# Performance work log

Hardware: AMD Instinct MI355X
Metric: run time of the kernel (lower is better)

Reference implementation:

```python
import jax, jax.numpy as jnp
import numpy as np

B, S, H = 32, 2048, 1024

def setup_inputs() -> dict:
    key = jax.random.key(0)
    k1, k2, k3, k4 = jax.random.split(key, 4)
    scale_w = 1.0 / np.sqrt(3 * H)
    scale_v = 1.0 / np.sqrt(H)
    return {
        "enc_output": jax.random.normal(k1, (B, S, 2 * H), dtype=jnp.float32),
        "enc_mask": jnp.ones((B, S, 1), dtype=jnp.float32),
        "dec_hidden": jax.random.normal(k2, (1, B, H), dtype=jnp.float32),
        "W_w": jax.random.normal(k3, (H, 3 * H), dtype=jnp.float32) * scale_w,
        "W_b": jnp.zeros((H,), dtype=jnp.float32),
        "V_w": jax.random.normal(k4, (1, H), dtype=jnp.float32) * scale_v,
        "V_b": jnp.zeros((1,), dtype=jnp.float32),
    }


def reference(enc_output, enc_mask, dec_hidden, W_w, W_b, V_w, V_b):
    # enc_output: (B, S, 2H); enc_mask: (B, S, 1); dec_hidden: (1, B, H)
    b, s, _ = enc_output.shape
    h = dec_hidden.shape[-1]
    dec = jnp.broadcast_to(jnp.transpose(dec_hidden, (1, 0, 2)), (b, s, h))  # (B,S,H)
    x = jnp.concatenate([enc_output, dec], axis=-1)                          # (B,S,3H)
    energy = jnp.tanh(jnp.einsum('bsk,hk->bsh', x, W_w) + W_b)               # (B,S,H)
    scores = jnp.einsum('bsh,oh->bso', energy, V_w)[..., 0] + V_b[0]         # (B,S)
    keep = enc_mask[..., 0] > 0  # original masks where (1 - mask) is True
    scores = jnp.where(keep, scores, -jnp.inf)
    attn = jax.nn.softmax(scores, axis=-1)                                   # (B,S)
    context = jnp.einsum('bs,bsd->bd', attn, enc_output)                     # (B,2H)
    return context
```

## Files before the change

### kernel.cpp

```cpp
#include <hip/hip_runtime.h>
#include <hip/hip_bf16.h>
#include <math.h>

#define B_   32
#define S_   2048
#define H_   1024
#define K2H  2048
#define M_TOT (B_*S_)

typedef __attribute__((ext_vector_type(8))) short bf16x8;
typedef __attribute__((ext_vector_type(4))) float f32x4;

__device__ __forceinline__ short f2bf(float f) {
    union { float f; unsigned u; } c; c.f = f;
    unsigned u = c.u;
    unsigned r = u + 0x7FFFu + ((u >> 16) & 1u);
    return (short)(r >> 16);
}

__device__ __forceinline__ void bar() {
    asm volatile("" ::: "memory");
    __builtin_amdgcn_s_barrier();
    asm volatile("" ::: "memory");
}

__device__ __forceinline__ void gload16(const short* g, short* l) {
    __builtin_amdgcn_global_load_lds(
        (const __attribute__((address_space(1))) void*)g,
        (__attribute__((address_space(3))) void*)l,
        16, 0, 0);
}

__global__ void prep_kernel(const float* __restrict__ enc, short* __restrict__ encb,
                            const float* __restrict__ Ww, short* __restrict__ w1,
                            const float* __restrict__ dec, const float* __restrict__ Wb,
                            float* __restrict__ dproj) {
    int bid = blockIdx.x;
    int t = threadIdx.x;
    if (bid < 65536) {
        size_t e = ((size_t)bid * 256 + t) * 8;
        float4 v0 = *reinterpret_cast<const float4*>(enc + e);
        float4 v1 = *reinterpret_cast<const float4*>(enc + e + 4);
        short s[8];
        s[0]=f2bf(v0.x); s[1]=f2bf(v0.y); s[2]=f2bf(v0.z); s[3]=f2bf(v0.w);
        s[4]=f2bf(v1.x); s[5]=f2bf(v1.y); s[6]=f2bf(v1.z); s[7]=f2bf(v1.w);
        *reinterpret_cast<int4*>(encb + e) = *reinterpret_cast<const int4*>(s);
    } else if (bid < 65536 + 2048) {
        int idx = (bid - 65536) * 256 + t;
        int e = idx * 4;
        int h = e >> 11;
        int k = e & 2047;
        float4 v = *reinterpret_cast<const float4*>(Ww + (size_t)h * 3072 + k);
        short4 o;
        o.x = f2bf(v.x); o.y = f2bf(v.y); o.z = f2bf(v.z); o.w = f2bf(v.w);
        *reinterpret_cast<short4*>(w1 + (size_t)h * 2048 + k) = o;
    } else {
        __shared__ float dl[1024];
        int db = bid - 65536 - 2048;
        int b = db >> 4;
        int hc = db & 15;
        for (int i = t; i < 1024; i += 256) dl[i] = dec[b * 1024 + i];
        __syncthreads();
        int wv = t >> 6, lane = t & 63;
        for (int it = 0; it < 16; ++it) {
            int h = hc * 64 + wv * 16 + it;
            const float* wrow = Ww + (size_t)h * 3072 + 2048;
            float acc = 0.f;
            for (int j = lane; j < 1024; j += 64) acc += dl[j] * wrow[j];
            for (int m = 32; m >= 1; m >>= 1) acc += __shfl_xor(acc, m);
            if (lane == 0) dproj[b * 1024 + h] = acc + Wb[h];
        }
    }
}

#define NT_ 64

#define STAGE(dst, src, T) do { \
    _Pragma("unroll") \
    for (int u = 0; u < 2; ++u) { \
        int lr = u * 128 + sr; \
        int cs = (sc ^ ((lr >> 1) & 3)) * 8; \
        gload16((src) + (size_t)lr * K2H + (T) * 32 + cs, (dst) + lr * 32 + sc * 8); \
    } } while (0)

#define RDA(dstf, AS, roff) do { \
    _Pragma("unroll") \
    for (int ii = 0; ii < 4; ++ii) { \
        int R = wm * 128 + (roff) + ii * 16 + (lane & 15); \
        dstf[ii] = *reinterpret_cast<const bf16x8*>(&(AS)[R * 32 + (((lane >> 4) ^ ((R >> 1) & 3)) * 8)]); \
    } } while (0)

#define RDB(dstf, BS) do { \
    _Pragma("unroll") \
    for (int jj = 0; jj < 4; ++jj) { \
        int R = wn * 64 + jj * 16 + (lane & 15); \
        dstf[jj] = *reinterpret_cast<const bf16x8*>(&(BS)[R * 32 + (((lane >> 4) ^ ((R >> 1) & 3)) * 8)]); \
    } } while (0)

#define TILE(T, AS, BS, APF, BPF) do { \
    RDA(aF, AS, 0); \
    RDB(bF, BS); \
    RDA(aG, AS, 64); \
    if ((T) + 3 < NT_) { STAGE(APF, abase, (T) + 3); STAGE(BPF, bbase, (T) + 3); } \
    if ((T) <= NT_ - 4)      { asm volatile("s_waitcnt vmcnt(8)" ::: "memory"); } \
    else if ((T) == NT_ - 3) { asm volatile("s_waitcnt vmcnt(4)" ::: "memory"); } \
    else if ((T) == NT_ - 2) { asm volatile("s_waitcnt vmcnt(0)" ::: "memory"); } \
    bar(); \
    __builtin_amdgcn_s_setprio(1); \
    _Pragma("unroll") for (int ii = 0; ii < 4; ++ii) \
      _Pragma("unroll") for (int jj = 0; jj < 4; ++jj) \
        acc[ii][jj] = __builtin_amdgcn_mfma_f32_16x16x32_bf16(aF[ii], bF[jj], acc[ii][jj], 0, 0, 0); \
    _Pragma("unroll") for (int ii = 0; ii < 4; ++ii) \
      _Pragma("unroll") for (int jj = 0; jj < 4; ++jj) \
        acc[4+ii][jj] = __builtin_amdgcn_mfma_f32_16x16x32_bf16(aG[ii], bF[jj], acc[4+ii][jj], 0, 0, 0); \
    __builtin_amdgcn_s_setprio(0); \
    bar(); \
} while (0)

__launch_bounds__(512, 1)
__global__ void fused_gemm8(const short* __restrict__ encb, const short* __restrict__ w1,
                            const float* __restrict__ dproj, const float* __restrict__ Vw,
                            float* __restrict__ scores_p) {
    __shared__ short A0[8192], A1[8192], A2[8192], A3[8192];
    __shared__ short B0[8192], B1[8192], B2[8192], B3[8192];
    int bid = blockIdx.x;
    int x = bid & 7, r = bid >> 3;
    int nt = r & 3;
    int mt = ((r >> 2) << 3) | x;
    int m0 = mt * 256, n0 = nt * 256;
    int t5 = threadIdx.x, lane = t5 & 63, wv = t5 >> 6;
    int wm = wv >> 2, wn = wv & 3;

    int sr = t5 >> 2;
    int sc = t5 & 3;
    const short* abase = encb + (size_t)m0 * K2H;
    const short* bbase = w1 + (size_t)n0 * K2H;

    f32x4 acc[8][4] = {};
    bf16x8 aF[4], aG[4], bF[4];

    STAGE(A0, abase, 0); STAGE(B0, bbase, 0);
    STAGE(A1, abase, 1); STAGE(B1, bbase, 1);
    STAGE(A2, abase, 2); STAGE(B2, bbase, 2);
    asm volatile("s_waitcnt vmcnt(8)" ::: "memory");
    bar();

    for (int to = 0; to < NT_ / 4; ++to) {
        int T = to * 4;
        TILE(T,     A0, B0, A3, B3);
        TILE(T + 1, A1, B1, A0, B0);
        TILE(T + 2, A2, B2, A1, B1);
        TILE(T + 3, A3, B3, A2, B2);
    }

    int b = m0 >> 11;
    float dp[4], vvv[4];
#pragma unroll
    for (int j = 0; j < 4; ++j) {
        int hg = n0 + wn * 64 + j * 16 + (lane & 15);
        dp[j] = dproj[b * 1024 + hg];
        vvv[j] = Vw[hg];
    }
    float* sp = scores_p + (size_t)(nt * 4 + wn) * M_TOT;
#pragma unroll
    for (int i = 0; i < 8; ++i) {
#pragma unroll
        for (int q = 0; q < 4; ++q) {
            float part = 0.f;
#pragma unroll
            for (int j = 0; j < 4; ++j)
                part += vvv[j] * tanhf(acc[i][j][q] + dp[j]);
            part += __shfl_xor(part, 1);
            part += __shfl_xor(part, 2);
            part += __shfl_xor(part, 4);
            part += __shfl_xor(part, 8);
            if ((lane & 15) == 0) {
                int mg = m0 + wm * 128 + i * 16 + ((lane >> 4) << 2) + q;
                sp[mg] = part;
            }
        }
    }
}

__global__ void softmax_kernel(const float* __restrict__ scores_p, const float* __restrict__ mask,
                               float* __restrict__ attn) {
    int b = blockIdx.x;
    int t = threadIdx.x;
    __shared__ float red[8];
    __shared__ float red2[8];
    float v[8];
    float mx = -INFINITY;
#pragma unroll
    for (int k = 0; k < 8; ++k) {
        int s = t + k * 256;
        float xv = 0.f;
#pragma unroll
        for (int p = 0; p < 16; ++p) xv += scores_p[(size_t)p * M_TOT + b * 2048 + s];
        float mk = mask[b * 2048 + s];
        xv = (mk > 0.f) ? xv : -INFINITY;
        v[k] = xv;
        mx = fmaxf(mx, xv);
    }
    int lane = t & 63, wv = t >> 6;
    for (int m = 32; m >= 1; m >>= 1) mx = fmaxf(mx, __shfl_xor(mx, m));
    if (lane == 0) red[wv] = mx;
    __syncthreads();
    mx = fmaxf(fmaxf(red[0], red[1]), fmaxf(red[2], red[3]));
    float sum = 0.f;
#pragma unroll
    for (int k = 0; k < 8; ++k) { v[k] = __expf(v[k] - mx); sum += v[k]; }
    for (int m = 32; m >= 1; m >>= 1) sum += __shfl_xor(sum, m);
    if (lane == 0) red2[wv] = sum;
    __syncthreads();
    sum = red2[0] + red2[1] + red2[2] + red2[3];
    float inv = 1.f / sum;
#pragma unroll
    for (int k = 0; k < 8; ++k) attn[b * 2048 + t + k * 256] = v[k] * inv;
}

#define SCH 64
__global__ void context_kernel(const short* __restrict__ encb, const float* __restrict__ attn,
                               float* __restrict__ out) {
    int bid = blockIdx.x;
    int b = bid >> 5;
    int schunk = bid & 31;
    int t = threadIdx.x;
    __shared__ float aw[SCH];
    if (t < SCH) aw[t] = attn[b * 2048 + schunk * SCH + t];
    __syncthreads();
    int c = t * 8;
    const short* base = encb + (size_t)b * S_ * K2H + (size_t)(schunk * SCH) * K2H + c;
    float acc[8] = {};
    for (int s = 0; s < SCH; ++s) {
        float w = aw[s];
        bf16x8 v = *reinterpret_cast<const bf16x8*>(base + (size_t)s * K2H);
#pragma unroll
        for (int j = 0; j < 8; ++j) {
            union { unsigned u; float f; } cv;
            cv.u = ((unsigned)(unsigned short)v[j]) << 16;
            acc[j] += w * cv.f;
        }
    }
    float* o = out + b * 2048 + c;
#pragma unroll
    for (int j = 0; j < 8; ++j) atomicAdd(o + j, acc[j]);
}

extern "C" void kernel_launch(void* const* d_in, const int* in_sizes, int n_in,
                              void* d_out, int out_size, void* d_ws, size_t ws_size,
                              hipStream_t stream) {
    const float* enc  = (const float*)d_in[0];
    const float* mask = (const float*)d_in[1];
    const float* dec  = (const float*)d_in[2];
    const float* Ww   = (const float*)d_in[3];
    const float* Wb   = (const float*)d_in[4];
    const float* Vw   = (const float*)d_in[5];
    float* out = (float*)d_out;

    char* ws = (char*)d_ws;
    const size_t ENC_B = (size_t)M_TOT * K2H * 2;
    short* encb     = (short*)ws;
    short* w1       = (short*)(ws + ENC_B);
    float* scores_p = (float*)(ws + ENC_B + (4u << 20));
    float* dproj    = (float*)(ws + ENC_B + (8u << 20));
    float* attn     = (float*)(ws + ENC_B + (8u << 20) + (128u << 10));

    hipMemsetAsync(out, 0, (size_t)out_size * sizeof(float), stream);

    prep_kernel<<<68096, 256, 0, stream>>>(enc, encb, Ww, w1, dec, Wb, dproj);
    fused_gemm8<<<1024, 512, 0, stream>>>(encb, w1, dproj, Vw, scores_p);
    softmax_kernel<<<32, 256, 0, stream>>>(scores_p, mask, attn);
    context_kernel<<<1024, 256, 0, stream>>>(encb, attn, out);
}
```

Before: 648.8 us.

## Interleave GEMM main loop into four MFMA phases with triple-buffered LDS

Restructures the bf16 GEMM main loop so each K-tile is split into four MFMA quadrants, with LDS fragment reads and global-to-LDS stage loads interleaved between barriers. The prefetch depth drops from three tiles ahead with four LDS buffers to two tiles ahead with three buffers, which cuts LDS usage. The aim is finer-grained overlap of memory traffic with MFMA work. The cost is more barriers per tile and less latency hiding from the shallower prefetch.

Result: slower. 679.6 us (+4.7%).

```diff
diff --git a/kernel.cpp b/kernel.cpp
--- a/kernel.cpp
+++ b/kernel.cpp
@@ -75,13 +75,11 @@
 
 #define NT_ 64
 
-#define STAGE(dst, src, T) do { \
-    _Pragma("unroll") \
-    for (int u = 0; u < 2; ++u) { \
-        int lr = u * 128 + sr; \
-        int cs = (sc ^ ((lr >> 1) & 3)) * 8; \
-        gload16((src) + (size_t)lr * K2H + (T) * 32 + cs, (dst) + lr * 32 + sc * 8); \
-    } } while (0)
+#define STAGE1(dst, src, T, RB) do { \
+    int gr_ = (RB) + sr; \
+    gload16((src) + (size_t)gr_ * K2H + (T) * 32 + ((sc ^ ((gr_ >> 1) & 3)) * 8), \
+            (dst) + gr_ * 32 + sc * 8); \
+  } while (0)
 
 #define RDA(dstf, AS, roff) do { \
     _Pragma("unroll") \
@@ -90,39 +88,48 @@
         dstf[ii] = *reinterpret_cast<const bf16x8*>(&(AS)[R * 32 + (((lane >> 4) ^ ((R >> 1) & 3)) * 8)]); \
     } } while (0)
 
-#define RDB(dstf, BS) do { \
+#define RDB2(dstf, BS, coff) do { \
     _Pragma("unroll") \
-    for (int jj = 0; jj < 4; ++jj) { \
-        int R = wn * 64 + jj * 16 + (lane & 15); \
+    for (int jj = 0; jj < 2; ++jj) { \
+        int R = wn * 64 + (coff) + jj * 16 + (lane & 15); \
         dstf[jj] = *reinterpret_cast<const bf16x8*>(&(BS)[R * 32 + (((lane >> 4) ^ ((R >> 1) & 3)) * 8)]); \
     } } while (0)
 
-#define TILE(T, AS, BS, APF, BPF) do { \
-    RDA(aF, AS, 0); \
-    RDB(bF, BS); \
-    RDA(aG, AS, 64); \
-    if ((T) + 3 < NT_) { STAGE(APF, abase, (T) + 3); STAGE(BPF, bbase, (T) + 3); } \
-    if ((T) <= NT_ - 4)      { asm volatile("s_waitcnt vmcnt(8)" ::: "memory"); } \
-    else if ((T) == NT_ - 3) { asm volatile("s_waitcnt vmcnt(4)" ::: "memory"); } \
-    else if ((T) == NT_ - 2) { asm volatile("s_waitcnt vmcnt(0)" ::: "memory"); } \
-    bar(); \
+#define MFMAQ(IO, JO, AFR, BFR) do { \
     __builtin_amdgcn_s_setprio(1); \
     _Pragma("unroll") for (int ii = 0; ii < 4; ++ii) \
-      _Pragma("unroll") for (int jj = 0; jj < 4; ++jj) \
-        acc[ii][jj] = __builtin_amdgcn_mfma_f32_16x16x32_bf16(aF[ii], bF[jj], acc[ii][jj], 0, 0, 0); \
-    _Pragma("unroll") for (int ii = 0; ii < 4; ++ii) \
-      _Pragma("unroll") for (int jj = 0; jj < 4; ++jj) \
-        acc[4+ii][jj] = __builtin_amdgcn_mfma_f32_16x16x32_bf16(aG[ii], bF[jj], acc[4+ii][jj], 0, 0, 0); \
+      _Pragma("unroll") for (int jj = 0; jj < 2; ++jj) \
+        acc[(IO)+ii][(JO)+jj] = __builtin_amdgcn_mfma_f32_16x16x32_bf16(AFR[ii], BFR[jj], acc[(IO)+ii][(JO)+jj], 0, 0, 0); \
     __builtin_amdgcn_s_setprio(0); \
-    bar(); \
-} while (0)
+  } while (0)
+
+#define TILE(T, AC, BC, APF, BPF) do { \
+    RDA(aF, AC, 0); \
+    RDB2(bF0, BC, 0); \
+    if ((T) + 2 < NT_) STAGE1(APF, abase, (T) + 2, 0); \
+    bar(); \
+    MFMAQ(0, 0, aF, bF0); \
+    RDB2(bF1, BC, 32); \
+    if ((T) + 2 < NT_) STAGE1(APF, abase, (T) + 2, 128); \
+    bar(); \
+    MFMAQ(0, 2, aF, bF1); \
+    RDA(aG, AC, 64); \
+    if ((T) + 2 < NT_) STAGE1(BPF, bbase, (T) + 2, 0); \
+    bar(); \
+    MFMAQ(4, 0, aG, bF0); \
+    if ((T) + 2 < NT_) STAGE1(BPF, bbase, (T) + 2, 128); \
+    if ((T) <= NT_ - 3)      { asm volatile("s_waitcnt vmcnt(4)" ::: "memory"); } \
+    else if ((T) == NT_ - 2) { asm volatile("s_waitcnt vmcnt(0)" ::: "memory"); } \
+    bar(); \
+    MFMAQ(4, 2, aG, bF1); \
+  } while (0)
 
 __launch_bounds__(512, 1)
 __global__ void fused_gemm8(const short* __restrict__ encb, const short* __restrict__ w1,
                             const float* __restrict__ dproj, const float* __restrict__ Vw,
                             float* __restrict__ scores_p) {
-    __shared__ short A0[8192], A1[8192], A2[8192], A3[8192];
-    __shared__ short B0[8192], B1[8192], B2[8192], B3[8192];
+    __shared__ short A0[8192], A1[8192], A2[8192];
+    __shared__ short B0[8192], B1[8192], B2[8192];
     int bid = blockIdx.x;
     int x = bid & 7, r = bid >> 3;
     int nt = r & 3;
@@ -137,21 +144,22 @@
     const short* bbase = w1 + (size_t)n0 * K2H;
 
     f32x4 acc[8][4] = {};
-    bf16x8 aF[4], aG[4], bF[4];
-
-    STAGE(A0, abase, 0); STAGE(B0, bbase, 0);
-    STAGE(A1, abase, 1); STAGE(B1, bbase, 1);
-    STAGE(A2, abase, 2); STAGE(B2, bbase, 2);
-    asm volatile("s_waitcnt vmcnt(8)" ::: "memory");
+    bf16x8 aF[4], aG[4], bF0[2], bF1[2];
+
+    STAGE1(A0, abase, 0, 0); STAGE1(A0, abase, 0, 128);
+    STAGE1(B0, bbase, 0, 0); STAGE1(B0, bbase, 0, 128);
+    STAGE1(A1, abase, 1, 0); STAGE1(A1, abase, 1, 128);
+    STAGE1(B1, bbase, 1, 0); STAGE1(B1, bbase, 1, 128);
+    asm volatile("s_waitcnt vmcnt(4)" ::: "memory");
     bar();
 
-    for (int to = 0; to < NT_ / 4; ++to) {
-        int T = to * 4;
-        TILE(T,     A0, B0, A3, B3);
+    for (int to = 0; to < 21; ++to) {
+        int T = to * 3;
+        TILE(T,     A0, B0, A2, B2);
         TILE(T + 1, A1, B1, A0, B0);
         TILE(T + 2, A2, B2, A1, B1);
-        TILE(T + 3, A3, B3, A2, B2);
-    }
+    }
+    TILE(63, A0, B0, A1, B1);
 
     int b = m0 >> 11;
     float dp[4], vvv[4];
```
